# Optimization experiments

Hardware: AMD Instinct MI355X
Metric: run time of the kernel (lower is better)

Reference implementation:

```python
import jax, jax.numpy as jnp
import numpy as np

B, N, E = 64, 512, 262144
D_EMB = 128   # 2 * embedding_dim
D_H = 128     # residue_emb_dim == iegmn_lay_hid_dim
L = 5         # iegmn_n_lays
X_INIT = 0.25 # residual mix toward original coords (IEGMN x_connection_init)


def silu(x):
    return x * jax.nn.sigmoid(x)


def _edges(k):
    # within-graph random edges: pick a graph, then a node inside it
    g = jax.random.randint(k, (E,), 0, B)
    n = jax.random.randint(jax.random.fold_in(k, 1), (E,), 0, N)
    return (g * N + n).astype(jnp.int32)


def setup_inputs() -> dict:
    key = jax.random.key(0)
    ks = jax.random.split(key, 16)
    Nt = B * N
    s = 0.05
    feat = jax.random.normal(ks[0], (Nt, D_EMB), jnp.float32)
    coords = jax.random.normal(ks[1], (Nt, 3), jnp.float32)
    c_valid = (jax.random.uniform(ks[2], (B, N)) > 0.3).astype(jnp.float32)
    c_valid = c_valid.at[:, 0].set(1.0)  # avoid empty graphs
    return {
        'feat': feat,
        'coords': coords,
        'c_valid': c_valid,
        'edge_src': _edges(ks[3]), 'edge_dst': _edges(ks[4]),
        'cross_src': _edges(ks[5]), 'cross_dst': _edges(ks[6]),
        'W_emb': jax.random.normal(ks[7], (D_H, D_EMB), jnp.float32) * s,
        'We1': jax.random.normal(ks[8], (L, 2 * D_H + 1, D_H), jnp.float32) * s,
        'be1': jnp.zeros((L, D_H), jnp.float32),
        'We2': jax.random.normal(ks[9], (L, D_H, D_H), jnp.float32) * s,
        'be2': jnp.zeros((L, D_H), jnp.float32),
        'Wx': jax.random.normal(ks[10], (L, D_H, 1), jnp.float32) * s,
        'Wh': jax.random.normal(ks[11], (L, 3 * D_H, D_H), jnp.float32) * s,
        'bh': jnp.zeros((L, D_H), jnp.float32),
        'Wfc': jax.random.normal(ks[12], (3, D_H, D_H), jnp.float32) * s,
        'bfc': jnp.zeros((3, D_H), jnp.float32),
        'Wout': jax.random.normal(ks[13], (D_H, 1), jnp.float32) * s,
        'bout': jnp.zeros((1,), jnp.float32),
    }


def _deg_inv(dst, n):
    deg = jax.ops.segment_sum(jnp.ones(dst.shape[0], jnp.float32), dst, num_segments=n)
    return (1.0 / jnp.maximum(deg, 1.0))[:, None]


def _iegmn_layer(p, src, dst, x, h, x0, h0, deg_inv):
    We1, be1, We2, be2, Wx, Wh, bh = p
    n = x.shape[0]
    dx = x[src] - x[dst]                                  # [E, 3]
    d2 = jnp.sum(dx * dx, -1, keepdims=True)              # [E, 1]
    m = silu(jnp.concatenate([h[src], h[dst], d2], -1) @ We1 + be1)
    m = silu(m @ We2 + be2)                               # [E, D_H]
    coef = jnp.tanh(m @ Wx)                               # [E, 1]
    agg_x = jax.ops.segment_sum(dx * coef, dst, num_segments=n) * deg_inv
    x_new = X_INIT * x0 + (1.0 - X_INIT) * x + agg_x
    agg_m = jax.ops.segment_sum(m, dst, num_segments=n) * deg_inv
    h_new = silu(jnp.concatenate([h, agg_m, h0], -1) @ Wh + bh)
    return x_new, h_new


def reference(feat, coords, c_valid, edge_src, edge_dst, cross_src, cross_dst,
              W_emb, We1, be1, We2, be2, Wx, Wh, bh, Wfc, bfc, Wout, bout):
    Nt = feat.shape[0]
    h = feat @ W_emb.T          # embede (no bias)
    h0, x0, x = h, coords, coords
    dgi = _deg_inv(edge_dst, Nt)
    dci = _deg_inv(cross_dst, Nt)
    for k in range(L):
        p = tuple(t[k] for t in (We1, be1, We2, be2, Wx, Wh, bh))
        # branch == 'both': run layer on graph then cross_graph with same input h
        x, c1 = _iegmn_layer(p, edge_src, edge_dst, x, h, x0, h0, dgi)
        x, c2 = _iegmn_layer(p, cross_src, cross_dst, x, h, x0, h0, dci)
        h = c2 - c1             # dropout is identity at inference
    # masked sum-pool / count
    hb = h.reshape(B, N, D_H)
    pooled = jnp.sum(hb * c_valid[..., None], axis=1) / jnp.sum(c_valid, axis=1, keepdims=True)
    z = pooled
    for i in range(Wfc.shape[0]):
        z = jax.nn.relu(z @ Wfc[i] + bfc[i])
    out = jax.nn.sigmoid(z @ Wout + bout)
    return out.reshape(-1)      # [B]
```

## Files before the change

### kernel.cpp

```cpp
#include <hip/hip_runtime.h>

#define DEVINL __device__ __forceinline__

constexpr int NT   = 32768;
constexpr int DH   = 128;
constexpr int NE   = 262144;
constexpr int BGR  = 64;
constexpr int NPG  = 512;
constexpr int LAYS = 5;
constexpr size_t LSTR = 32768*3 + 98304;

typedef __attribute__((ext_vector_type(8))) short bf16x8;
typedef __attribute__((ext_vector_type(4))) float f32x4;
typedef __attribute__((ext_vector_type(4))) unsigned int uint4v;
typedef unsigned int uint;

DEVINL float siluf(float v){ return v * (1.0f/(1.0f + __expf(-v))); }
DEVINL float tanh_fast(float x){ float e = __expf(2.0f*x); return 1.0f - 2.0f/(e + 1.0f); }

DEVINL uint bf16_rne(float f){
  uint x = __float_as_uint(f);
  return (x + 0x7fffu + ((x>>16)&1u)) >> 16;
}

DEVINL void split8(const float* m, bf16x8& h, bf16x8& l){
  #pragma unroll
  for (int j=0;j<8;j++){
    uint x  = __float_as_uint(m[j]);
    uint hb = x >> 16;
    float hf = __uint_as_float(hb<<16);
    uint lb = bf16_rne(m[j] - hf);
    h[j] = (short)hb; l[j] = (short)lb;
  }
}

DEVINL f32x4 mma3(bf16x8 ah, bf16x8 al, bf16x8 bh, bf16x8 bl, f32x4 acc){
  acc = __builtin_amdgcn_mfma_f32_16x16x32_bf16(al, bh, acc, 0,0,0);
  acc = __builtin_amdgcn_mfma_f32_16x16x32_bf16(ah, bl, acc, 0,0,0);
  acc = __builtin_amdgcn_mfma_f32_16x16x32_bf16(ah, bh, acc, 0,0,0);
  return acc;
}

#define GLOAD_LDS16(g, l) __builtin_amdgcn_global_load_lds( \
    (const __attribute__((address_space(1))) void*)(g), \
    (__attribute__((address_space(3))) void*)(l), 16, 0, 0)

__global__ __launch_bounds__(256) void k_prep_all(
    const float* __restrict__ W_emb, const float* __restrict__ We1,
    const float* __restrict__ We2,  const float* __restrict__ Wh,
    short* __restrict__ wemb_p, short* __restrict__ lay_p)
{
  const int idx = blockIdx.x*256 + threadIdx.x;
  const float* src; short* dst; int v; bool trans = false;
  if (idx < 16384){ src = W_emb; dst = wemb_p; v = idx; trans = true; }
  else {
    const int u = idx - 16384;
    const int layer = u / 98304;
    const int w = u - layer*98304;
    short* p = lay_p + (size_t)layer*LSTR;
    if (w < 16384)      { src = We1 + (size_t)layer*257*DH;          dst = p;         v = w; }
    else if (w < 32768) { src = We1 + (size_t)layer*257*DH + 128*DH; dst = p + 32768; v = w - 16384; }
    else if (w < 49152) { src = We2 + (size_t)layer*DH*DH;           dst = p + 65536; v = w - 32768; }
    else                { src = Wh  + (size_t)layer*3*DH*DH;         dst = p + 98304; v = w - 49152; }
  }
  const int k = v>>7, col = v&127;
  const float val = trans ? src[(size_t)col*128 + k] : src[(size_t)k*128 + col];
  uint hb = __float_as_uint(val) >> 16;
  float hf = __uint_as_float(hb<<16);
  uint lb = bf16_rne(val - hf);
  const int kc = k>>5, q = (k&31)>>3, j = k&7;
  const size_t o = (size_t)kc*8192 + q*1024 + col*8 + j;
  dst[o]        = (short)hb;
  dst[o + 4096] = (short)lb;
}

__global__ __launch_bounds__(256) void k_hist2(const int* __restrict__ edst,
                                               const int* __restrict__ cdst,
                                               int* __restrict__ cnt){
  const int half = blockIdx.x >= (NE/256);
  const int e = (blockIdx.x - half*(NE/256))*256 + threadIdx.x;
  const int* d = half ? cdst : edst;
  atomicAdd(&cnt[half*NT + d[e]], 1);
}

__global__ __launch_bounds__(1024) void k_scan2(const int* __restrict__ cnt,
                                                int* __restrict__ cur,
                                                float* __restrict__ dinv){
  __shared__ int part[1024];
  const int off = blockIdx.x * NT;
  const int tid = threadIdx.x;
  const int base = tid*32;
  int s = 0;
  for (int i=0;i<32;i++){
    const int c = cnt[off + base + i];
    dinv[off + base + i] = 1.0f / (float)(c > 1 ? c : 1);
    s += c;
  }
  const int own = s;
  part[tid] = s; __syncthreads();
  for (int o=1; o<1024; o<<=1){
    int v = (tid>=o) ? part[tid-o] : 0;
    __syncthreads();
    part[tid] += v;
    __syncthreads();
  }
  int run = part[tid] - own;
  for (int i=0;i<32;i++){ cur[off + base + i] = run; run += cnt[off + base + i]; }
}

__global__ __launch_bounds__(256) void k_scatter2(const int* __restrict__ esrc,
                                                  const int* __restrict__ edst,
                                                  const int* __restrict__ csrc,
                                                  const int* __restrict__ cdst,
                                                  int* __restrict__ cur,
                                                  int2* __restrict__ sd){
  const int half = blockIdx.x >= (NE/256);
  const int e = (blockIdx.x - half*(NE/256))*256 + threadIdx.x;
  const int* sA = half ? csrc : esrc;
  const int* dA = half ? cdst : edst;
  const int dv = dA[e];
  const int p = atomicAdd(&cur[half*NT + dv], 1);
  int2 v; v.x = sA[e]; v.y = dv;
  sd[half*NE + p] = v;
}

template<int MODE>
__global__ __launch_bounds__(512) void k_ngemm(
    const float* __restrict__ A0, float* __restrict__ A1, const float* __restrict__ A2,
    const float* __restrict__ dinv, const short* __restrict__ W0, const short* __restrict__ W1,
    const float* __restrict__ bias, const float* __restrict__ c1in,
    float* __restrict__ out0, float* __restrict__ out1)
{
  const int tid = threadIdx.x;
  const int wv = tid>>6, lane = tid&63, c = lane&15, q = lane>>4;
  const int rowt = wv & 3, grp = wv >> 2;
  const int row = blockIdx.x*64 + rowt*16 + c;
  constexpr int KC = (MODE>=2) ? 12 : 4;
  constexpr int TT = (MODE==1) ? 8 : 4;
  float dv = 1.0f;
  if constexpr (MODE>=2) dv = dinv[row];
  const short* Wp = W0;
  if constexpr (MODE==1){ if (grp==1) Wp = W1; }
  f32x4 acc[TT];
  #pragma unroll
  for (int t=0;t<TT;t++){ acc[t][0]=0.f; acc[t][1]=0.f; acc[t][2]=0.f; acc[t][3]=0.f; }

  #pragma unroll
  for (int kc=0; kc<KC; ++kc){
    const float* asrc = A0; float sc = 1.0f;
    if constexpr (MODE>=2){
      if (kc >= 8)      { asrc = A2; }
      else if (kc >= 4) { asrc = A1; sc = dv; }
    }
    const int koff = (kc&3)*32 + q*8;
    float4 v0 = *(const float4*)(asrc + (size_t)row*128 + koff);
    float4 v1 = *(const float4*)(asrc + (size_t)row*128 + koff + 4);
    float m[8] = {v0.x*sc,v0.y*sc,v0.z*sc,v0.w*sc,v1.x*sc,v1.y*sc,v1.z*sc,v1.w*sc};
    bf16x8 ah, al; split8(m, ah, al);
    #pragma unroll
    for (int t=0;t<TT;t++){
      const int tg = (MODE==1) ? t : grp*4 + t;
      const short* fp = Wp + (size_t)kc*8192 + q*1024 + (tg*16 + c)*8;
      bf16x8 bh = *(const bf16x8*)fp;
      bf16x8 bl = *(const bf16x8*)(fp + 4096);
      acc[t] = mma3(ah, al, bh, bl, acc[t]);
    }
  }
  #pragma unroll
  for (int t=0;t<TT;t++){
    const int tg = (MODE==1) ? t : grp*4 + t;
    const int col = tg*16 + c;
    float b0 = 0.f;
    if constexpr (MODE==1){ if (grp==0) b0 = bias[col]; }
    else if constexpr (MODE>=2){ b0 = bias[col]; }
    #pragma unroll
    for (int r=0;r<4;r++){
      const size_t orow = (size_t)blockIdx.x*64 + rowt*16 + q*4 + r;
      float v = acc[t][r];
      if constexpr (MODE==0){
        out0[orow*128 + col] = v; out1[orow*128 + col] = v;
      } else if constexpr (MODE==1){
        if (grp==0) out0[orow*128 + col] = v + b0;
        else        out1[orow*128 + col] = v;
      } else if constexpr (MODE==2){
        out0[orow*128 + col] = siluf(v + b0);
      } else {
        out0[orow*128 + col] = siluf(v + b0) - c1in[orow*128 + col];
      }
    }
  }
  if constexpr (MODE>=2){
    __syncthreads();
    float4 z; z.x=0.f; z.y=0.f; z.z=0.f; z.w=0.f;
    float4* zp = (float4*)(A1 + (size_t)blockIdx.x*64*128);
    #pragma unroll
    for (int i=0;i<4;i++) zp[tid + i*512] = z;
  }
}

__global__ __launch_bounds__(512, 4) void k_edge(
    const int2* __restrict__ sd, const float* __restrict__ x,
    const float* __restrict__ Aw, const float* __restrict__ Bw,
    const short* __restrict__ w2p, const float* __restrict__ We1_l,
    const float* __restrict__ be2_l, const float* __restrict__ Wx_l,
    float* __restrict__ aggm, float* __restrict__ aggx)
{
  __shared__ __align__(16) short w2t[32768];
  __shared__ __align__(16) float w256s[128];
  __shared__ __align__(16) float wxs[128];
  __shared__ __align__(16) float be2s[128];
  __shared__ float dxs[8][16][3];
  __shared__ int   dsts[8][16];
  const int tid = threadIdx.x;
  const int wv = tid>>6, lane = tid&63, c = lane&15, q = lane>>4;
  const int er = wv*16 + c;
  const int2 sdv = sd[blockIdx.x*128 + er];
  #pragma unroll
  for (int i=0;i<8;i++)
    GLOAD_LDS16(w2p + (size_t)(tid + i*512)*8, w2t + (size_t)(wv*64 + i*512)*8);
  if (tid < 128){ w256s[tid]=We1_l[256*128+tid]; wxs[tid]=Wx_l[tid]; be2s[tid]=be2_l[tid]; }
  const int s = sdv.x, d = sdv.y;
  const float xs0=x[s*3+0], xs1=x[s*3+1], xs2=x[s*3+2];
  const float xd0=x[d*3+0], xd1=x[d*3+1], xd2=x[d*3+2];
  const float* ap = Aw + (size_t)s*128 + q*8;
  const float* bp = Bw + (size_t)d*128 + q*8;
  float4 aa[8], bb[8];
  #pragma unroll
  for (int kc=0;kc<4;kc++){
    aa[2*kc]   = *(const float4*)(ap + kc*32);
    aa[2*kc+1] = *(const float4*)(ap + kc*32 + 4);
    bb[2*kc]   = *(const float4*)(bp + kc*32);
    bb[2*kc+1] = *(const float4*)(bp + kc*32 + 4);
  }
  const float dx0 = xs0-xd0, dx1 = xs1-xd1, dx2 = xs2-xd2;
  const float d2  = dx0*dx0 + dx1*dx1 + dx2*dx2;
  if (q==0){ dxs[wv][c][0]=dx0; dxs[wv][c][1]=dx1; dxs[wv][c][2]=dx2; dsts[wv][c]=d; }
  __syncthreads();

  bf16x8 ah[4], al[4];
  #pragma unroll
  for (int kc=0;kc<4;kc++){
    const int kb = kc*32 + q*8;
    float4 w0 = *(const float4*)&w256s[kb], w1 = *(const float4*)&w256s[kb+4];
    float4 av0=aa[2*kc], av1=aa[2*kc+1], bv0=bb[2*kc], bv1=bb[2*kc+1];
    float m[8];
    m[0]=siluf(av0.x+bv0.x+d2*w0.x); m[1]=siluf(av0.y+bv0.y+d2*w0.y);
    m[2]=siluf(av0.z+bv0.z+d2*w0.z); m[3]=siluf(av0.w+bv0.w+d2*w0.w);
    m[4]=siluf(av1.x+bv1.x+d2*w1.x); m[5]=siluf(av1.y+bv1.y+d2*w1.y);
    m[6]=siluf(av1.z+bv1.z+d2*w1.z); m[7]=siluf(av1.w+bv1.w+d2*w1.w);
    split8(m, ah[kc], al[kc]);
  }

  const int rb = q*4;
  const int rd0 = dsts[wv][rb+0], rd1 = dsts[wv][rb+1];
  const int rd2 = dsts[wv][rb+2], rd3 = dsts[wv][rb+3];
  const bool b1 = (rd1!=rd0), b2 = (rd2!=rd1), b3 = (rd3!=rd2);

  float pd[4] = {0.f, 0.f, 0.f, 0.f};
  #pragma unroll
  for (int gi=0; gi<2; ++gi){
    f32x4 acc[4];
    #pragma unroll
    for (int tt=0;tt<4;tt++){ acc[tt][0]=0.f; acc[tt][1]=0.f; acc[tt][2]=0.f; acc[tt][3]=0.f; }
    #pragma unroll
    for (int kc=0;kc<4;kc++){
      #pragma unroll
      for (int tt=0;tt<4;tt++){
        const int col = (gi*4+tt)*16 + c;
        const short* fp = &w2t[kc*8192 + q*1024 + col*8];
        bf16x8 bh = *(const bf16x8*)fp;
        bf16x8 bl = *(const bf16x8*)(fp + 4096);
        acc[tt] = mma3(ah[kc], al[kc], bh, bl, acc[tt]);
      }
    }
    #pragma unroll
    for (int tt=0;tt<4;tt++){
      const int col = (gi*4+tt)*16 + c;
      const float be = be2s[col], wx = wxs[col];
      #pragma unroll
      for (int r=0;r<4;r++){
        float v = siluf(acc[tt][r] + be);
        acc[tt][r] = v;
        pd[r] += v*wx;
      }
      float v3 = acc[tt][3];
      float v2 = acc[tt][2] + (b3 ? 0.f : v3);
      float v1 = acc[tt][1] + (b2 ? 0.f : v2);
      float v0 = acc[tt][0] + (b1 ? 0.f : v1);
      unsafeAtomicAdd(aggm + (size_t)rd0*128 + col, v0);
      if (b1) unsafeAtomicAdd(aggm + (size_t)rd1*128 + col, v1);
      if (b2) unsafeAtomicAdd(aggm + (size_t)rd2*128 + col, v2);
      if (b3) unsafeAtomicAdd(aggm + (size_t)rd3*128 + col, v3);
    }
  }
  #pragma unroll
  for (int msk=1; msk<16; msk<<=1){
    #pragma unroll
    for (int r=0;r<4;r++) pd[r] += __shfl_xor(pd[r], msk);
  }
  if (c < 3){
    float a0 = dxs[wv][rb+0][c]*tanh_fast(pd[0]);
    float a1 = dxs[wv][rb+1][c]*tanh_fast(pd[1]);
    float a2 = dxs[wv][rb+2][c]*tanh_fast(pd[2]);
    float a3 = dxs[wv][rb+3][c]*tanh_fast(pd[3]);
    float v3 = a3;
    float v2 = a2 + (b3 ? 0.f : v3);
    float v1 = a1 + (b2 ? 0.f : v2);
    float v0 = a0 + (b1 ? 0.f : v1);
    unsafeAtomicAdd(aggx + (size_t)rd0*3 + c, v0);
    if (b1) unsafeAtomicAdd(aggx + (size_t)rd1*3 + c, v1);
    if (b2) unsafeAtomicAdd(aggx + (size_t)rd2*3 + c, v2);
    if (b3) unsafeAtomicAdd(aggx + (size_t)rd3*3 + c, v3);
  }
}

__global__ __launch_bounds__(256) void k_xupd(float* __restrict__ x, const float* __restrict__ x0,
                                              float* __restrict__ aggx,
                                              const float* __restrict__ dinv){
  int i = blockIdx.x*256 + threadIdx.x;
  if (i < NT*3){
    int n = i/3;
    x[i] = 0.25f*x0[i] + 0.75f*x[i] + aggx[i]*dinv[n];
    aggx[i] = 0.f;
  }
}

__global__ __launch_bounds__(512) void k_pool(const float* __restrict__ h,
                                              const float* __restrict__ cvalid,
                                              float* __restrict__ pooled){
  __shared__ float red[4][128];
  __shared__ float redc[4];
  const int b = blockIdx.x, t = threadIdx.x, j = t&127, sl = t>>7;
  float s = 0.f, cf = 0.f;
  for (int n=sl; n<NPG; n+=4){
    const float m = cvalid[b*NPG + n];
    s  += h[((size_t)b*NPG + n)*DH + j] * m;
    cf += m;
  }
  red[sl][j] = s;
  if (j==0) redc[sl] = cf;
  __syncthreads();
  if (t < 128){
    float ss = red[0][t]+red[1][t]+red[2][t]+red[3][t];
    float cc = redc[0]+redc[1]+redc[2]+redc[3];
    pooled[b*DH + t] = ss / cc;
  }
}

__global__ __launch_bounds__(256) void k_mlp(const float* __restrict__ pooled,
                                             const float* __restrict__ Wfc,
                                             const float* __restrict__ bfc,
                                             const float* __restrict__ Wout,
                                             const float* __restrict__ bout,
                                             float* __restrict__ out)
{
  __shared__ __align__(16) float z[64*132];
  __shared__ __align__(16) float wB[128*128];
  const int t = threadIdx.x;
  {
    const int n = t>>2, qq = t&3;
    const float4* p = (const float4*)(pooled + n*DH + qq*32);
    float4* w = (float4*)&z[n*132 + qq*32];
    #pragma unroll
    for (int u=0;u<8;u++) w[u] = p[u];
  }
  const int g = t>>5, lane = t&31, c0 = lane*4;
  for (int l=0;l<3;l++){
    #pragma unroll
    for (int i=0;i<16;i++){
      const int idx = t + i*256;
      ((float4*)wB)[idx] = ((const float4*)(Wfc + (size_t)l*DH*DH))[idx];
    }
    __syncthreads();
    float acc[8][4];
    #pragma unroll
    for (int i=0;i<8;i++){ acc[i][0]=0.f; acc[i][1]=0.f; acc[i][2]=0.f; acc[i][3]=0.f; }
    #pragma unroll 4
    for (int kk=0; kk<128; kk+=4){
      float4 b0=*(const float4*)&wB[(kk+0)*128+c0];
      float4 b1=*(const float4*)&wB[(kk+1)*128+c0];
      float4 b2=*(const float4*)&wB[(kk+2)*128+c0];
      float4 b3=*(const float4*)&wB[(kk+3)*128+c0];
      #pragma unroll
      for (int i=0;i<8;i++){
        float4 a=*(const float4*)&z[(g*8+i)*132 + kk];
        acc[i][0]+=a.x*b0.x+a.y*b1.x+a.z*b2.x+a.w*b3.x;
        acc[i][1]+=a.x*b0.y+a.y*b1.y+a.z*b2.y+a.w*b3.y;
        acc[i][2]+=a.x*b0.z+a.y*b1.z+a.z*b2.z+a.w*b3.z;
        acc[i][3]+=a.x*b0.w+a.y*b1.w+a.z*b2.w+a.w*b3.w;
      }
    }
    __syncthreads();
    #pragma unroll
    for (int i=0;i<8;i++){
      float v0=acc[i][0]+bfc[l*DH+c0+0]; v0 = v0>0.f?v0:0.f;
      float v1=acc[i][1]+bfc[l*DH+c0+1]; v1 = v1>0.f?v1:0.f;
      float v2=acc[i][2]+bfc[l*DH+c0+2]; v2 = v2>0.f?v2:0.f;
      float v3=acc[i][3]+bfc[l*DH+c0+3]; v3 = v3>0.f?v3:0.f;
      float4 v; v.x=v0; v.y=v1; v.z=v2; v.w=v3;
      *(float4*)&z[(g*8+i)*132 + c0] = v;
    }
    __syncthreads();
  }
  if (t < 64){
    float a = 0.f;
    for (int k2=0;k2<128;k2++) a += z[t*132 + k2]*Wout[k2];
    out[t] = 1.0f/(1.0f + __expf(-(a + bout[0])));
  }
}

extern "C" void kernel_launch(void* const* d_in, const int* in_sizes, int n_in,
                              void* d_out, int out_size, void* d_ws, size_t ws_size,
                              hipStream_t stream)
{
  (void)in_sizes; (void)n_in; (void)out_size; (void)ws_size;
  const float* feat   = (const float*)d_in[0];
  const float* coords = (const float*)d_in[1];
  const float* cvalid = (const float*)d_in[2];
  const int*   esrc   = (const int*)d_in[3];
  const int*   edst   = (const int*)d_in[4];
  const int*   csrc   = (const int*)d_in[5];
  const int*   cdst   = (const int*)d_in[6];
  const float* W_emb  = (const float*)d_in[7];
  const float* We1    = (const float*)d_in[8];
  const float* be1    = (const float*)d_in[9];
  const float* We2    = (const float*)d_in[10];
  const float* be2    = (const float*)d_in[11];
  const float* Wx     = (const float*)d_in[12];
  const float* Wh     = (const float*)d_in[13];
  const float* bh     = (const float*)d_in[14];
  const float* Wfc    = (const float*)d_in[15];
  const float* bfc    = (const float*)d_in[16];
  const float* Wout   = (const float*)d_in[17];
  const float* bout   = (const float*)d_in[18];

  float* ws = (float*)d_ws;
  float* h      = ws; ws += (size_t)NT*DH;
  float* h0     = ws; ws += (size_t)NT*DH;
  float* c1     = ws; ws += (size_t)NT*DH;
  float* Aw     = ws; ws += (size_t)NT*DH;
  float* Bw     = ws; ws += (size_t)NT*DH;
  float* aggm   = ws; ws += (size_t)NT*DH;
  float* aggx   = ws; ws += (size_t)NT*3;
  float* x      = ws; ws += (size_t)NT*3;
  float* dgi    = ws; ws += NT;
  float* dci    = ws; ws += NT;
  float* pooled = ws; ws += BGR*DH;
  int2* sdG   = (int2*)ws; ws += (size_t)4*NE;
  int* cnt    = (int*)c1;
  int* cursor = cnt + 2*NT;
  short* pst    = (short*)ws;
  short* wemb_p = pst;
  short* lay_p  = pst + 32768;

  hipMemsetAsync(aggm, 0, (size_t)NT*(DH+3)*sizeof(float), stream);

  k_prep_all<<<1984, 256, 0, stream>>>(W_emb, We1, We2, Wh, wemb_p, lay_p);

  hipMemsetAsync(cnt, 0, 2*NT*sizeof(int), stream);
  k_hist2   <<<2*(NE/256), 256, 0, stream>>>(edst, cdst, cnt);
  k_scan2   <<<2, 1024, 0, stream>>>(cnt, cursor, dgi);
  k_scatter2<<<2*(NE/256), 256, 0, stream>>>(esrc, edst, csrc, cdst, cursor, sdG);

  k_ngemm<0><<<NT/64, 512, 0, stream>>>(feat, nullptr, nullptr, nullptr,
                                        wemb_p, nullptr, nullptr, nullptr, h, h0);
  hipMemcpyAsync(x, coords, (size_t)NT*3*sizeof(float), hipMemcpyDeviceToDevice, stream);

  for (int k=0; k<LAYS; k++){
    short* p = lay_p + (size_t)k*LSTR;
    const float* We1_l = We1 + (size_t)k*257*DH;
    const float* be1_l = be1 + (size_t)k*DH;
    const float* be2_l = be2 + (size_t)k*DH;
    const float* Wx_l  = Wx  + (size_t)k*DH;
    const float* bh_l  = bh  + (size_t)k*DH;

    k_ngemm<1><<<NT/64, 512, 0, stream>>>(h, nullptr, nullptr, nullptr,
                                          p, p + 32768, be1_l, nullptr, Aw, Bw);
    k_edge<<<NE/128, 512, 0, stream>>>(sdG, x, Aw, Bw,
                                       p + 65536, We1_l, be2_l, Wx_l, aggm, aggx);
    k_xupd<<<(NT*3+255)/256, 256, 0, stream>>>(x, coords, aggx, dgi);
    k_ngemm<2><<<NT/64, 512, 0, stream>>>(h, aggm, h0, dgi,
                                          p + 98304, nullptr, bh_l, nullptr, c1, nullptr);
    k_edge<<<NE/128, 512, 0, stream>>>(sdG + NE, x, Aw, Bw,
                                       p + 65536, We1_l, be2_l, Wx_l, aggm, aggx);
    k_xupd<<<(NT*3+255)/256, 256, 0, stream>>>(x, coords, aggx, dci);
    k_ngemm<3><<<NT/64, 512, 0, stream>>>(h, aggm, h0, dci,
                                          p + 98304, nullptr, bh_l, c1, h, nullptr);
  }

  k_pool<<<BGR, 512, 0, stream>>>(h, cvalid, pooled);
  k_mlp <<<1, 256, 0, stream>>>(pooled, Wfc, bfc, Wout, bout, (float*)d_out);
}
```

Baseline: 1.724 ms.

## Halve edge-kernel LDS by reading low-half weights from global, raise occupancy

The edge kernel now keeps only the high bf16 half of the We2 split weights in shared memory (32KB instead of 64KB) and reads the low half straight from global/L2. The launch bound goes from 4 to 8 blocks per CU. The A/B gather loads are folded into the k-loop so no 64-float register prefetch is held, and all 8 column tiles accumulate at once. The aim is more resident waves to hide gather and atomic latency, at the cost of extra global traffic for the low-half weights and 32 accumulator registers live at the same time.

```diff
diff --git a/kernel.cpp b/kernel.cpp
--- a/kernel.cpp
+++ b/kernel.cpp
@@ -198,14 +198,14 @@
   }
 }
 
-__global__ __launch_bounds__(512, 4) void k_edge(
+__global__ __launch_bounds__(512, 8) void k_edge(
     const int2* __restrict__ sd, const float* __restrict__ x,
     const float* __restrict__ Aw, const float* __restrict__ Bw,
     const short* __restrict__ w2p, const float* __restrict__ We1_l,
     const float* __restrict__ be2_l, const float* __restrict__ Wx_l,
     float* __restrict__ aggm, float* __restrict__ aggx)
 {
-  __shared__ __align__(16) short w2t[32768];
+  __shared__ __align__(16) short w2t[16384];
   __shared__ __align__(16) float w256s[128];
   __shared__ __align__(16) float wxs[128];
   __shared__ __align__(16) float be2s[128];
@@ -216,82 +216,65 @@
   const int er = wv*16 + c;
   const int2 sdv = sd[blockIdx.x*128 + er];
   #pragma unroll
-  for (int i=0;i<8;i++)
-    GLOAD_LDS16(w2p + (size_t)(tid + i*512)*8, w2t + (size_t)(wv*64 + i*512)*8);
+  for (int i=0;i<4;i++)
+    GLOAD_LDS16(w2p + (size_t)i*8192 + tid*8, w2t + i*4096 + wv*512);
   if (tid < 128){ w256s[tid]=We1_l[256*128+tid]; wxs[tid]=Wx_l[tid]; be2s[tid]=be2_l[tid]; }
   const int s = sdv.x, d = sdv.y;
   const float xs0=x[s*3+0], xs1=x[s*3+1], xs2=x[s*3+2];
   const float xd0=x[d*3+0], xd1=x[d*3+1], xd2=x[d*3+2];
-  const float* ap = Aw + (size_t)s*128 + q*8;
-  const float* bp = Bw + (size_t)d*128 + q*8;
-  float4 aa[8], bb[8];
-  #pragma unroll
-  for (int kc=0;kc<4;kc++){
-    aa[2*kc]   = *(const float4*)(ap + kc*32);
-    aa[2*kc+1] = *(const float4*)(ap + kc*32 + 4);
-    bb[2*kc]   = *(const float4*)(bp + kc*32);
-    bb[2*kc+1] = *(const float4*)(bp + kc*32 + 4);
-  }
   const float dx0 = xs0-xd0, dx1 = xs1-xd1, dx2 = xs2-xd2;
   const float d2  = dx0*dx0 + dx1*dx1 + dx2*dx2;
   if (q==0){ dxs[wv][c][0]=dx0; dxs[wv][c][1]=dx1; dxs[wv][c][2]=dx2; dsts[wv][c]=d; }
   __syncthreads();
 
-  bf16x8 ah[4], al[4];
-  #pragma unroll
-  for (int kc=0;kc<4;kc++){
+  const float* ap = Aw + (size_t)s*128 + q*8;
+  const float* bp = Bw + (size_t)d*128 + q*8;
+  const short* lo = w2p + 4096 + q*1024 + c*8;
+  f32x4 acc[8];
+  #pragma unroll
+  for (int t=0;t<8;t++){ acc[t][0]=0.f; acc[t][1]=0.f; acc[t][2]=0.f; acc[t][3]=0.f; }
+  #pragma unroll
+  for (int kc=0; kc<4; ++kc){
     const int kb = kc*32 + q*8;
-    float4 w0 = *(const float4*)&w256s[kb], w1 = *(const float4*)&w256s[kb+4];
-    float4 av0=aa[2*kc], av1=aa[2*kc+1], bv0=bb[2*kc], bv1=bb[2*kc+1];
+    float4 av0 = *(const float4*)(ap + kc*32), av1 = *(const float4*)(ap + kc*32 + 4);
+    float4 bv0 = *(const float4*)(bp + kc*32), bv1 = *(const float4*)(bp + kc*32 + 4);
+    float4 w0  = *(const float4*)&w256s[kb],   w1  = *(const float4*)&w256s[kb+4];
     float m[8];
     m[0]=siluf(av0.x+bv0.x+d2*w0.x); m[1]=siluf(av0.y+bv0.y+d2*w0.y);
     m[2]=siluf(av0.z+bv0.z+d2*w0.z); m[3]=siluf(av0.w+bv0.w+d2*w0.w);
     m[4]=siluf(av1.x+bv1.x+d2*w1.x); m[5]=siluf(av1.y+bv1.y+d2*w1.y);
     m[6]=siluf(av1.z+bv1.z+d2*w1.z); m[7]=siluf(av1.w+bv1.w+d2*w1.w);
-    split8(m, ah[kc], al[kc]);
-  }
-
+    bf16x8 ah, al; split8(m, ah, al);
+    #pragma unroll
+    for (int t=0;t<8;t++){
+      bf16x8 bh = *(const bf16x8*)&w2t[kc*4096 + q*1024 + (t*16 + c)*8];
+      bf16x8 bl = *(const bf16x8*)(lo + (size_t)kc*8192 + t*128);
+      acc[t] = mma3(ah, al, bh, bl, acc[t]);
+    }
+  }
   const int rb = q*4;
   const int rd0 = dsts[wv][rb+0], rd1 = dsts[wv][rb+1];
   const int rd2 = dsts[wv][rb+2], rd3 = dsts[wv][rb+3];
   const bool b1 = (rd1!=rd0), b2 = (rd2!=rd1), b3 = (rd3!=rd2);
-
   float pd[4] = {0.f, 0.f, 0.f, 0.f};
   #pragma unroll
-  for (int gi=0; gi<2; ++gi){
-    f32x4 acc[4];
-    #pragma unroll
-    for (int tt=0;tt<4;tt++){ acc[tt][0]=0.f; acc[tt][1]=0.f; acc[tt][2]=0.f; acc[tt][3]=0.f; }
-    #pragma unroll
-    for (int kc=0;kc<4;kc++){
-      #pragma unroll
-      for (int tt=0;tt<4;tt++){
-        const int col = (gi*4+tt)*16 + c;
-        const short* fp = &w2t[kc*8192 + q*1024 + col*8];
-        bf16x8 bh = *(const bf16x8*)fp;
-        bf16x8 bl = *(const bf16x8*)(fp + 4096);
-        acc[tt] = mma3(ah[kc], al[kc], bh, bl, acc[tt]);
-      }
-    }
-    #pragma unroll
-    for (int tt=0;tt<4;tt++){
-      const int col = (gi*4+tt)*16 + c;
-      const float be = be2s[col], wx = wxs[col];
-      #pragma unroll
-      for (int r=0;r<4;r++){
-        float v = siluf(acc[tt][r] + be);
-        acc[tt][r] = v;
-        pd[r] += v*wx;
-      }
-      float v3 = acc[tt][3];
-      float v2 = acc[tt][2] + (b3 ? 0.f : v3);
-      float v1 = acc[tt][1] + (b2 ? 0.f : v2);
-      float v0 = acc[tt][0] + (b1 ? 0.f : v1);
-      unsafeAtomicAdd(aggm + (size_t)rd0*128 + col, v0);
-      if (b1) unsafeAtomicAdd(aggm + (size_t)rd1*128 + col, v1);
-      if (b2) unsafeAtomicAdd(aggm + (size_t)rd2*128 + col, v2);
-      if (b3) unsafeAtomicAdd(aggm + (size_t)rd3*128 + col, v3);
-    }
+  for (int t=0;t<8;t++){
+    const int col = t*16 + c;
+    const float be = be2s[col], wx = wxs[col];
+    #pragma unroll
+    for (int r=0;r<4;r++){
+      float v = siluf(acc[t][r] + be);
+      acc[t][r] = v;
+      pd[r] += v*wx;
+    }
+    float v3 = acc[t][3];
+    float v2 = acc[t][2] + (b3 ? 0.f : v3);
+    float v1 = acc[t][1] + (b2 ? 0.f : v2);
+    float v0 = acc[t][0] + (b1 ? 0.f : v1);
+    unsafeAtomicAdd(aggm + (size_t)rd0*128 + col, v0);
+    if (b1) unsafeAtomicAdd(aggm + (size_t)rd1*128 + col, v1);
+    if (b2) unsafeAtomicAdd(aggm + (size_t)rd2*128 + col, v2);
+    if (b3) unsafeAtomicAdd(aggm + (size_t)rd3*128 + col, v3);
   }
   #pragma unroll
   for (int msk=1; msk<16; msk<<=1){
```

Result: slower. 2.007 ms (+16.4%).
